# Kernel optimization log

Measured on AMD Instinct MI355X. Metric: run time of the kernel, lower is better.

The kernel has to match this reference:

```python
import jax, jax.numpy as jnp
import numpy as np

B, L, D, H = 2, 2048, 768, 12
DH = D // H          # 64
DFF = 4 * D          # 3072
ALPHA = 0.25         # lorentz_alpha
BLEND = 0.5          # blend for FFN and MinkowskiLayerNorm (set via set_blend)
EPS = 1e-5
SCALE = float(np.sqrt(DH))


def setup_inputs() -> dict:
    key = jax.random.key(0)
    ks = jax.random.split(key, 14)
    w = lambda k, shape: jax.random.normal(k, shape, jnp.float32) * 0.02
    causal = jnp.tril(jnp.ones((L, L), bool))
    attention_mask = jnp.where(causal, 0.0, -1e9).astype(jnp.float32)[None, None]
    return {
        'x': jax.random.normal(ks[0], (B, L, D), jnp.float32),
        'attention_mask': attention_mask,
        'timelike_mask': jax.random.bernoulli(ks[1], 0.25, (D,)),
        'Wq': w(ks[2], (D, D)), 'Wk': w(ks[3], (D, D)),
        'Wv': w(ks[4], (D, D)), 'Wo': w(ks[5], (D, D)),
        'w1': w(ks[6], (DFF, D)), 'w2': w(ks[7], (D, DFF)),
        'w1_t': w(ks[8], (DFF // 2, D)), 'w2_t': w(ks[9], (D, DFF // 2)),
        'w1_s': w(ks[10], (DFF // 2, D)), 'w2_s': w(ks[11], (D, DFF // 2)),
        'n1_w': jnp.ones(D, jnp.float32), 'n1_b': jnp.zeros(D, jnp.float32),
        'n2_w': jnp.ones(D, jnp.float32), 'n2_b': jnp.zeros(D, jnp.float32),
    }


def _mink_norm(x, m, w, b):
    # Minkowski LayerNorm blended with standard LN (m: float timelike mask)
    mean = x.mean(-1, keepdims=True)
    xc = x - mean
    var = (xc * xc).mean(-1, keepdims=True)
    x_std = xc / jnp.sqrt(var + EPS)
    sq = xc * xc
    eta = (sq * (1.0 - m)).sum(-1, keepdims=True) - (sq * m).sum(-1, keepdims=True)
    x_eta = xc / jnp.sqrt(jnp.abs(eta) + EPS)
    xn = (1.0 - BLEND) * x_std + BLEND * x_eta
    return w * xn + b


def _attn(x, attention_mask, m, Wq, Wk, Wv, Wo):
    # (B,L,D) -> (B,H,L,DH)
    split = lambda t: t.reshape(B, L, H, DH).transpose(0, 2, 1, 3)
    Q = split(x @ Wq.T)
    K = split(x @ Wk.T)
    V = split(x @ Wv.T)
    scores = jnp.einsum('bhqd,bhkd->bhqk', Q, K) / SCALE
    # Minkowski timelike correction: per-head diagonal mask on Q
    m2 = m.reshape(H, DH)[None, :, None, :]          # (1,H,1,DH)
    Q_t = Q * m2
    q_norm = jnp.linalg.norm(Q, axis=-1, keepdims=True)
    qt_norm = jnp.linalg.norm(Q_t, axis=-1, keepdims=True)
    sf = jnp.where(qt_norm > 1e-6, q_norm / jnp.maximum(qt_norm, 1e-8), 0.0)
    time_inner = jnp.einsum('bhqd,bhkd->bhqk', Q_t * sf, K) / SCALE
    scores = scores - 2.0 * ALPHA * time_inner
    scores = scores + attention_mask
    aw = jax.nn.softmax(scores, axis=-1)
    out = jnp.einsum('bhqk,bhkd->bhqd', aw, V)
    out = out.transpose(0, 2, 1, 3).reshape(B, L, D)
    return out @ Wo.T


def _ffn(x, m, w1, w2, w1_t, w2_t, w1_s, w2_s):
    std_out = jax.nn.gelu(x @ w1.T, approximate=False) @ w2.T
    h_t = jax.nn.silu((x * m) @ w1_t.T) @ w2_t.T
    h_s = jax.nn.gelu((x * (1.0 - m)) @ w1_s.T, approximate=False) @ w2_s.T
    return (1.0 - BLEND) * std_out + BLEND * (h_t + h_s)


def reference(x, attention_mask, timelike_mask, Wq, Wk, Wv, Wo,
              w1, w2, w1_t, w2_t, w1_s, w2_s, n1_w, n1_b, n2_w, n2_b):
    m = timelike_mask.astype(jnp.float32)
    ao = _attn(_mink_norm(x, m, n1_w, n1_b), attention_mask, m, Wq, Wk, Wv, Wo)
    x = x + ao
    x = x + _ffn(_mink_norm(x, m, n2_w, n2_b), m, w1, w2, w1_t, w2_t, w1_s, w2_s)
    return x
```

## Files before the change

### kernel.cpp

```cpp
#include <hip/hip_runtime.h>


typedef unsigned short u16;
typedef __bf16 bfrag __attribute__((ext_vector_type(8)));
typedef float f32x4 __attribute__((ext_vector_type(4)));

#define MFMA(a, b, c) __builtin_amdgcn_mfma_f32_16x16x32_bf16(a, b, c, 0, 0, 0)
#define NEG_BIG (-30000.0f)
#define ASYNC16(g, l)                                                        \
  __builtin_amdgcn_global_load_lds(                                          \
      (const __attribute__((address_space(1))) unsigned int*)(g),            \
      (__attribute__((address_space(3))) unsigned int*)(l), 16, 0, 0)

__device__ __forceinline__ float bf2f(u16 u) {
  unsigned int v = ((unsigned int)u) << 16;
  float f; __builtin_memcpy(&f, &v, 4); return f;
}
__device__ __forceinline__ u16 f2bf(float f) {
  unsigned int v; __builtin_memcpy(&v, &f, 4);
  v += 0x7fffu + ((v >> 16) & 1u);
  return (u16)(v >> 16);
}
__device__ __forceinline__ bfrag ldfrag(const u16* p) {
  bfrag v; __builtin_memcpy(&v, p, 16); return v;
}

__global__ __launch_bounds__(256) void mask_conv_k(const void* __restrict__ mask,
                                                   float* __restrict__ mfl) {
  __shared__ int msh;
  if (threadIdx.x == 0) msh = 0;
  __syncthreads();
  const unsigned int* w = (const unsigned int*)mask;
  if (threadIdx.x < 192) {
    const unsigned int v = w[threadIdx.x];
    if ((v & 0xFFFFu) == 0x3F80u) atomicOr(&msh, 4);
    else if (v == 0x3F800000u) atomicOr(&msh, 2);
    else if (v >= 2u) atomicOr(&msh, 1);
  }
  __syncthreads();
  const int m = msh;
  const int mode = (m & 4) ? 3 : (m & 2) ? 2 : (m & 1) ? 1 : 0;
  for (int i = threadIdx.x; i < 768; i += 256) {
    int b;
    if (mode == 3) b = ((const u16*)mask)[i] != 0;
    else if (mode == 2) b = ((const float*)mask)[i] != 0.0f;
    else if (mode == 1) b = ((const unsigned char*)mask)[i] != 0;
    else b = ((const int*)mask)[i] != 0;
    mfl[i] = (float)b;
  }
}

struct Segs {
  const void* src[14];
  int off[14];
  int n[14];
  int mmode[14];
};

__global__ __launch_bounds__(256) void convert_k(Segs segs, u16* __restrict__ dstb,
                                                 const float* __restrict__ mfl) {
  const int seg = blockIdx.y;
  const int n = segs.n[seg];
  const int mm = segs.mmode[seg];
  u16* dst = dstb + segs.off[seg];
  const float* src = (const float*)segs.src[seg];
  for (int i = (blockIdx.x * 256 + threadIdx.x) * 4; i < n; i += gridDim.x * 1024) {
    float4 v;
    __builtin_memcpy(&v, src + i, 16);
    if (mm) {
      const int k = i % 768;
      float m0 = mfl[k], m1 = mfl[k + 1], m2 = mfl[k + 2], m3 = mfl[k + 3];
      if (mm == 2) { m0 = 1.f - m0; m1 = 1.f - m1; m2 = 1.f - m2; m3 = 1.f - m3; }
      v.x *= m0; v.y *= m1; v.z *= m2; v.w *= m3;
    }
    dst[i] = f2bf(v.x); dst[i + 1] = f2bf(v.y);
    dst[i + 2] = f2bf(v.z); dst[i + 3] = f2bf(v.w);
  }
}

__global__ __launch_bounds__(256) void mink_norm_k(
    const float* __restrict__ X, const float* __restrict__ mf,
    const u16* __restrict__ w, const u16* __restrict__ bias,
    u16* __restrict__ Y) {
  __shared__ float red[8];
  const int row = blockIdx.x, tid = threadIdx.x;
  const int wid = tid >> 6, lane = tid & 63;
  const size_t roff = (size_t)row * 768;

  float xv[3], mv[3];
  int idx[3];
#pragma unroll
  for (int i = 0; i < 3; i++) {
    idx[i] = tid + i * 256;
    xv[i] = X[roff + idx[i]];
    mv[i] = mf[idx[i]];
  }
  float s = xv[0] + xv[1] + xv[2];
#pragma unroll
  for (int o = 32; o >= 1; o >>= 1) s += __shfl_xor(s, o, 64);
  if (lane == 0) red[wid] = s;
  __syncthreads();
  const float mean = (red[0] + red[1] + red[2] + red[3]) * (1.0f / 768.0f);
  __syncthreads();

  float xc[3], ss = 0.0f, sm = 0.0f;
#pragma unroll
  for (int i = 0; i < 3; i++) {
    xc[i] = xv[i] - mean;
    ss += xc[i] * xc[i];
    sm += xc[i] * xc[i] * mv[i];
  }
#pragma unroll
  for (int o = 32; o >= 1; o >>= 1) {
    ss += __shfl_xor(ss, o, 64);
    sm += __shfl_xor(sm, o, 64);
  }
  if (lane == 0) { red[wid] = ss; red[4 + wid] = sm; }
  __syncthreads();
  const float sumsq = red[0] + red[1] + red[2] + red[3];
  const float summ = red[4] + red[5] + red[6] + red[7];
  const float var = sumsq * (1.0f / 768.0f);
  const float eta = sumsq - 2.0f * summ;
  const float rs = 1.0f / sqrtf(var + 1e-5f);
  const float re = 1.0f / sqrtf(fabsf(eta) + 1e-5f);

#pragma unroll
  for (int i = 0; i < 3; i++) {
    const float xn = xc[i] * 0.5f * (rs + re);
    Y[roff + idx[i]] = f2bf(bf2f(w[idx[i]]) * xn + bf2f(bias[idx[i]]));
  }
}

__global__ __launch_bounds__(256) void qcorr_k(u16* __restrict__ Q,
                                               const float* __restrict__ mf) {
  const int idx = blockIdx.x * 4 + (threadIdx.x >> 6);
  const int t = threadIdx.x & 63;
  const int h = idx % 12;
  const int bl = idx / 12;
  const size_t off = (size_t)bl * 768 + h * 64 + t;
  const float q = bf2f(Q[off]);
  const float m = mf[h * 64 + t];
  float q2 = q * q, qm2 = q * q * m;
#pragma unroll
  for (int o = 32; o >= 1; o >>= 1) {
    q2 += __shfl_xor(q2, o, 64);
    qm2 += __shfl_xor(qm2, o, 64);
  }
  const float qn = sqrtf(q2), qtn = sqrtf(qm2);
  const float sf = (qtn > 1e-6f) ? qn / fmaxf(qtn, 1e-8f) : 0.0f;
  Q[off] = f2bf(q * (1.0f - 0.5f * sf * m) * 0.125f);
}

__device__ __forceinline__ void gemm128_loop(
    const u16* __restrict__ Ab, const u16* __restrict__ Wb2,
    int K, int lda, int ldb, u16 (*As)[32], u16 (*Bs)[32], f32x4 acc[4][4]) {
  const int tid = threadIdx.x;
  const int wid = tid >> 6, lane = tid & 63;
  const int lr = lane & 15, lq = lane >> 4;
  const int srow = wid * 32 + (lane >> 2);
  const int scol = (lane & 3) * 8;
  const u16* ga0 = Ab + (size_t)srow * lda + scol;
  const u16* ga1 = Ab + (size_t)(srow + 16) * lda + scol;
  const u16* gb0 = Wb2 + (size_t)srow * ldb + scol;
  const u16* gb1 = Wb2 + (size_t)(srow + 16) * ldb + scol;
  u16* la0 = &As[wid * 32][0];
  u16* la1 = &As[wid * 32 + 16][0];
  u16* lb0 = &Bs[wid * 32][0];
  u16* lb1 = &Bs[wid * 32 + 16][0];
  const int wr = (wid >> 1) * 64, wc = (wid & 1) * 64;

  for (int k0 = 0; k0 < K; k0 += 32) {
    __syncthreads();
    ASYNC16(ga0 + k0, la0);
    ASYNC16(ga1 + k0, la1);
    ASYNC16(gb0 + k0, lb0);
    ASYNC16(gb1 + k0, lb1);
    __syncthreads();
    bfrag af[4], bf4[4];
#pragma unroll
    for (int i = 0; i < 4; i++) af[i] = ldfrag(&As[wr + i * 16 + lr][lq * 8]);
#pragma unroll
    for (int j = 0; j < 4; j++) bf4[j] = ldfrag(&Bs[wc + j * 16 + lr][lq * 8]);
#pragma unroll
    for (int i = 0; i < 4; i++)
#pragma unroll
      for (int j = 0; j < 4; j++)
        acc[i][j] = MFMA(af[i], bf4[j], acc[i][j]);
  }
}

struct GSeg { const u16* W; u16* C; int ldc; int nblk; int epi; };
struct GArgs { GSeg s[3]; };

__global__ __launch_bounds__(256) void gemm128_fused(
    const u16* __restrict__ A, int lda, int K, GArgs args) {
  __shared__ __align__(16) u16 As[128][32];
  __shared__ __align__(16) u16 Bs[128][32];
  int cb = blockIdx.x, seg = 0;
  while (cb >= args.s[seg].nblk) { cb -= args.s[seg].nblk; seg++; }
  const GSeg g = args.s[seg];
  const int rowb = blockIdx.y * 128, colb = cb * 128;
  f32x4 acc[4][4] = {};
  gemm128_loop(A + (size_t)rowb * lda, g.W + (size_t)colb * K, K, lda, K,
               As, Bs, acc);

  const int lane = threadIdx.x & 63, wid = threadIdx.x >> 6;
  const int lr = lane & 15, lq = lane >> 4;
  const int wr = (wid >> 1) * 64, wc = (wid & 1) * 64;
#pragma unroll
  for (int i = 0; i < 4; i++)
#pragma unroll
    for (int j = 0; j < 4; j++)
#pragma unroll
      for (int r = 0; r < 4; r++) {
        const int row = rowb + wr + i * 16 + lq * 4 + r;
        const int col = colb + wc + j * 16 + lr;
        float v = acc[i][j][r];
        if (g.epi == 2) v = 0.5f * v * (1.0f + erff(v * 0.70710678118654752f));
        else if (g.epi == 3) v = v / (1.0f + __expf(-v));
        g.C[(size_t)row * g.ldc + col] = f2bf(v);
      }
}

__global__ __launch_bounds__(256) void gemm128_res(
    const u16* __restrict__ A, const u16* __restrict__ W,
    const float* __restrict__ R, float* __restrict__ Out, int lda, int K,
    int N) {
  __shared__ __align__(16) u16 As[128][32];
  __shared__ __align__(16) u16 Bs[128][32];
  const int rowb = blockIdx.y * 128, colb = blockIdx.x * 128;
  f32x4 acc[4][4] = {};
  gemm128_loop(A + (size_t)rowb * lda, W + (size_t)colb * K, K, lda, K,
               As, Bs, acc);

  const int lane = threadIdx.x & 63, wid = threadIdx.x >> 6;
  const int lr = lane & 15, lq = lane >> 4;
  const int wr = (wid >> 1) * 64, wc = (wid & 1) * 64;
#pragma unroll
  for (int i = 0; i < 4; i++)
#pragma unroll
    for (int j = 0; j < 4; j++)
#pragma unroll
      for (int r = 0; r < 4; r++) {
        const int row = rowb + wr + i * 16 + lq * 4 + r;
        const int col = colb + wc + j * 16 + lr;
        const size_t o = (size_t)row * N + col;
        Out[o] = acc[i][j][r] + R[o];
      }
}

__global__ __launch_bounds__(256) void ffn2_splitk(
    const u16* __restrict__ H1, const u16* __restrict__ Ht,
    const u16* __restrict__ Hs, const u16* __restrict__ W2,
    const u16* __restrict__ W2t, const u16* __restrict__ W2s,
    float* __restrict__ Out) {
  __shared__ __align__(16) u16 As[128][32];
  __shared__ __align__(16) u16 Bs[128][32];
  const int rowb = blockIdx.y * 128, colb = blockIdx.x * 128;
  const int z = blockIdx.z;
  f32x4 acc[4][4] = {};
  if (z == 0)
    gemm128_loop(H1 + (size_t)rowb * 3072, W2 + (size_t)colb * 3072,
                 1536, 3072, 3072, As, Bs, acc);
  else if (z == 1)
    gemm128_loop(H1 + (size_t)rowb * 3072 + 1536,
                 W2 + (size_t)colb * 3072 + 1536,
                 1536, 3072, 3072, As, Bs, acc);
  else if (z == 2)
    gemm128_loop(Ht + (size_t)rowb * 1536, W2t + (size_t)colb * 1536,
                 1536, 1536, 1536, As, Bs, acc);
  else
    gemm128_loop(Hs + (size_t)rowb * 1536, W2s + (size_t)colb * 1536,
                 1536, 1536, 1536, As, Bs, acc);

  const int lane = threadIdx.x & 63, wid = threadIdx.x >> 6;
  const int lr = lane & 15, lq = lane >> 4;
  const int wr = (wid >> 1) * 64, wc = (wid & 1) * 64;
#pragma unroll
  for (int i = 0; i < 4; i++)
#pragma unroll
    for (int j = 0; j < 4; j++)
#pragma unroll
      for (int r = 0; r < 4; r++) {
        const int row = rowb + wr + i * 16 + lq * 4 + r;
        const int col = colb + wc + j * 16 + lr;
        atomicAdd(&Out[(size_t)row * 768 + col], 0.5f * acc[i][j][r]);
      }
}

__global__ __launch_bounds__(256) void flash_attn_k(
    const u16* __restrict__ Qc, const u16* __restrict__ Kb,
    const u16* __restrict__ Vb, u16* __restrict__ O) {
  __shared__ __align__(16) u16 Ks[64][40];
  __shared__ __align__(16) u16 Vt[64][72];
  __shared__ __align__(16) u16 Ps[4][16][72];
  const int tid = threadIdx.x, wid = tid >> 6, lane = tid & 63;
  const int lr = lane & 15, lq = lane >> 4;
  const int qt = gridDim.x - 1 - blockIdx.x;
  const int qb = qt * 64;
  const int bh = blockIdx.y;
  const int b = bh / 12, h = bh % 12;
  const int q0 = qb + wid * 16;
  const size_t base = (size_t)b * 2048 * 768 + h * 64;

  bfrag aq[2];
  aq[0] = ldfrag(Qc + base + (size_t)(q0 + lr) * 768 + lq * 8);
  aq[1] = ldfrag(Qc + base + (size_t)(q0 + lr) * 768 + 32 + lq * 8);

  f32x4 o[4] = {};
  float mrow[4] = {NEG_BIG, NEG_BIG, NEG_BIG, NEG_BIG};
  float lrow[4] = {0.0f, 0.0f, 0.0f, 0.0f};

  const int krow = tid >> 3;
  const int kcol = (tid & 7) * 8;
  const int vkey = tid & 31;
  const int vdg = tid >> 5;

  const int nt = qt + 1;

  const u16* kp = Kb + base + (size_t)krow * 768 + kcol;
  const u16* vp = Vb + base + (size_t)vkey * 768 + vdg * 8;

  uint4 kv0, kv1, vv0, vv1;
  __builtin_memcpy(&kv0, kp, 16);
  __builtin_memcpy(&kv1, kp + (size_t)32 * 768, 16);
  __builtin_memcpy(&vv0, vp, 16);
  __builtin_memcpy(&vv1, vp + (size_t)32 * 768, 16);

  for (int kt = 0; kt < nt; kt++) {
    __syncthreads();
    __builtin_memcpy(&Ks[krow][kcol], &kv0, 16);
    __builtin_memcpy(&Ks[krow + 32][kcol], &kv1, 16);
    {
      union { uint4 u; u16 s[8]; } a, b2;
      a.u = vv0; b2.u = vv1;
#pragma unroll
      for (int j = 0; j < 8; j++) {
        Vt[vdg * 8 + j][vkey] = a.s[j];
        Vt[vdg * 8 + j][vkey + 32] = b2.s[j];
      }
    }
    __syncthreads();
    if (kt + 1 < nt) {
      const size_t koff = (size_t)(kt + 1) * 64 * 768;
      __builtin_memcpy(&kv0, kp + koff, 16);
      __builtin_memcpy(&kv1, kp + koff + (size_t)32 * 768, 16);
      __builtin_memcpy(&vv0, vp + koff, 16);
      __builtin_memcpy(&vv1, vp + koff + (size_t)32 * 768, 16);
    }

    const int kbk = kt * 64;
    if (kbk <= q0 + 15) {
      f32x4 s4[4] = {};
#pragma unroll
      for (int kg = 0; kg < 2; kg++) {
#pragma unroll
        for (int c = 0; c < 4; c++) {
          bfrag bk = ldfrag(&Ks[c * 16 + lr][kg * 32 + lq * 8]);
          s4[c] = MFMA(aq[kg], bk, s4[c]);
        }
      }
#pragma unroll
      for (int r = 0; r < 4; r++) {
        const int q = q0 + lq * 4 + r;
        float v[4];
        float mx = NEG_BIG;
#pragma unroll
        for (int c = 0; c < 4; c++) {
          v[c] = (kbk + c * 16 + lr > q) ? NEG_BIG : s4[c][r];
          mx = fmaxf(mx, v[c]);
        }
#pragma unroll
        for (int off = 8; off >= 1; off >>= 1)
          mx = fmaxf(mx, __shfl_xor(mx, off, 16));
        const float mn = fmaxf(mrow[r], mx);
        const float alpha = __expf(mrow[r] - mn);
        float sm = 0.0f;
        float p[4];
#pragma unroll
        for (int c = 0; c < 4; c++) {
          p[c] = __expf(v[c] - mn);
          sm += p[c];
        }
#pragma unroll
        for (int off = 8; off >= 1; off >>= 1) sm += __shfl_xor(sm, off, 16);
        lrow[r] = lrow[r] * alpha + sm;
        mrow[r] = mn;
#pragma unroll
        for (int dt = 0; dt < 4; dt++) o[dt][r] *= alpha;
#pragma unroll
        for (int c = 0; c < 4; c++)
          Ps[wid][lq * 4 + r][c * 16 + lr] = f2bf(p[c]);
      }
      __threadfence_block();
      bfrag pf0 = ldfrag(&Ps[wid][lr][lq * 8]);
      bfrag pf1 = ldfrag(&Ps[wid][lr][32 + lq * 8]);
#pragma unroll
      for (int dt = 0; dt < 4; dt++) {
        bfrag v0 = ldfrag(&Vt[dt * 16 + lr][lq * 8]);
        bfrag v1 = ldfrag(&Vt[dt * 16 + lr][32 + lq * 8]);
        o[dt] = MFMA(pf0, v0, o[dt]);
        o[dt] = MFMA(pf1, v1, o[dt]);
      }
    }
  }

#pragma unroll
  for (int r = 0; r < 4; r++) {
    const float inv = 1.0f / fmaxf(lrow[r], 1e-30f);
    const int q = q0 + lq * 4 + r;
#pragma unroll
    for (int dt = 0; dt < 4; dt++)
      O[base + (size_t)q * 768 + dt * 16 + lr] = f2bf(o[dt][r] * inv);
  }
}

extern "C" void kernel_launch(void* const* d_in, const int* in_sizes, int n_in,
                              void* d_out, int out_size, void* d_ws,
                              size_t ws_size, hipStream_t stream) {
  (void)in_sizes; (void)n_in; (void)out_size; (void)ws_size;
  const float* x = (const float*)d_in[0];
  const void* mask = d_in[2];

  char* ws = (char*)d_ws;
  u16* Wb  = (u16*)(ws);
  u16* n1h = (u16*)(ws + 23599104);
  u16* Qb  = (u16*)(ws + 48764928);
  u16* Kb2 = (u16*)(ws + 55056384);
  u16* Vb2 = (u16*)(ws + 61347840);
  u16* att = (u16*)(ws + 67639296);
  u16* hs  = (u16*)(ws + 80222208);
  float* mfl = (float*)(ws + 92805120);
  float* x1 = (float*)d_out;

  u16* Wq = Wb + 0,        *Wk = Wb + 589824,   *Wv = Wb + 1179648;
  u16* Wo = Wb + 1769472,  *w1 = Wb + 2359296,  *w1t = Wb + 4718592;
  u16* w1s = Wb + 5898240, *w2 = Wb + 7077888,  *w2t = Wb + 9437184;
  u16* w2s = Wb + 10616832;
  u16* n1w = Wb + 11796480, *n1b = Wb + 11797248;
  u16* n2w = Wb + 11798016, *n2b = Wb + 11798784;

  Segs sg;
  const int srcidx[14] = {3, 4, 5, 6, 7, 9, 11, 8, 10, 12, 13, 14, 15, 16};
  const int offs[14] = {0, 589824, 1179648, 1769472, 2359296, 4718592,
                        5898240, 7077888, 9437184, 10616832,
                        11796480, 11797248, 11798016, 11798784};
  const int ns[14] = {589824, 589824, 589824, 589824, 2359296, 1179648,
                      1179648, 2359296, 1179648, 1179648, 768, 768, 768, 768};
  const int mms[14] = {0, 0, 0, 0, 0, 1, 2, 0, 0, 0, 0, 0, 0, 0};
  for (int i = 0; i < 14; i++) {
    sg.src[i] = d_in[srcidx[i]];
    sg.off[i] = offs[i];
    sg.n[i] = ns[i];
    sg.mmode[i] = mms[i];
  }

  mask_conv_k<<<1, 256, 0, stream>>>(mask, mfl);
  convert_k<<<dim3(2304, 14), 256, 0, stream>>>(sg, Wb, mfl);

  mink_norm_k<<<4096, 256, 0, stream>>>(x, mfl, n1w, n1b, n1h);

  GArgs qkv;
  qkv.s[0] = {Wq, Qb, 768, 6, 0};
  qkv.s[1] = {Wk, Kb2, 768, 6, 0};
  qkv.s[2] = {Wv, Vb2, 768, 6, 0};
  gemm128_fused<<<dim3(18, 32), 256, 0, stream>>>(n1h, 768, 768, qkv);

  qcorr_k<<<12288, 256, 0, stream>>>(Qb, mfl);
  flash_attn_k<<<dim3(32, 24), 256, 0, stream>>>(Qb, Kb2, Vb2, att);

  gemm128_res<<<dim3(6, 32), 256, 0, stream>>>(att, Wo, x, x1, 768, 768, 768);

  mink_norm_k<<<4096, 256, 0, stream>>>(x1, mfl, n2w, n2b, Qb);

  GArgs ffn1;
  ffn1.s[0] = {w1, n1h, 3072, 24, 2};
  ffn1.s[1] = {w1t, att, 1536, 12, 3};
  ffn1.s[2] = {w1s, hs, 1536, 12, 2};
  gemm128_fused<<<dim3(48, 32), 256, 0, stream>>>(Qb, 768, 768, ffn1);

  ffn2_splitk<<<dim3(6, 32, 4), 256, 0, stream>>>(n1h, att, hs, w2, w2t, w2s,
                                                  (float*)d_out);
}
```

Before: 465.4 us.

## Halve flash-attention query tile and split-K the Wo projection with atomics

Flash attention now runs 128-thread blocks over 32 query rows, launching twice as many blocks so the causal workload balances better across CUs. Each thread loads twice as much K/V data per tile to compensate for the smaller block. The Wo projection is split along K into two halves that atomically accumulate into x1. The residual is pre-seeded by having the first norm kernel copy x into x1. This raises parallelism for the small GEMM, at the cost of extra atomic traffic, nondeterministic summation order, and each K/V tile being loaded twice as often overall.

```diff
diff --git a/kernel.cpp b/kernel.cpp
--- a/kernel.cpp
+++ b/kernel.cpp
@@ -81,7 +81,7 @@
 __global__ __launch_bounds__(256) void mink_norm_k(
     const float* __restrict__ X, const float* __restrict__ mf,
     const u16* __restrict__ w, const u16* __restrict__ bias,
-    u16* __restrict__ Y) {
+    u16* __restrict__ Y, float* __restrict__ Xcopy) {
   __shared__ float red[8];
   const int row = blockIdx.x, tid = threadIdx.x;
   const int wid = tid >> 6, lane = tid & 63;
@@ -94,6 +94,10 @@
     idx[i] = tid + i * 256;
     xv[i] = X[roff + idx[i]];
     mv[i] = mf[idx[i]];
+  }
+  if (Xcopy) {
+#pragma unroll
+    for (int i = 0; i < 3; i++) Xcopy[roff + idx[i]] = xv[i];
   }
   float s = xv[0] + xv[1] + xv[2];
 #pragma unroll
@@ -222,16 +226,16 @@
       }
 }
 
-__global__ __launch_bounds__(256) void gemm128_res(
+__global__ __launch_bounds__(256) void gemm128_wo_splitk(
     const u16* __restrict__ A, const u16* __restrict__ W,
-    const float* __restrict__ R, float* __restrict__ Out, int lda, int K,
-    int N) {
+    float* __restrict__ Out) {
   __shared__ __align__(16) u16 As[128][32];
   __shared__ __align__(16) u16 Bs[128][32];
   const int rowb = blockIdx.y * 128, colb = blockIdx.x * 128;
+  const int z = blockIdx.z;
   f32x4 acc[4][4] = {};
-  gemm128_loop(A + (size_t)rowb * lda, W + (size_t)colb * K, K, lda, K,
-               As, Bs, acc);
+  gemm128_loop(A + (size_t)rowb * 768 + z * 384,
+               W + (size_t)colb * 768 + z * 384, 384, 768, 768, As, Bs, acc);
 
   const int lane = threadIdx.x & 63, wid = threadIdx.x >> 6;
   const int lr = lane & 15, lq = lane >> 4;
@@ -244,8 +248,7 @@
       for (int r = 0; r < 4; r++) {
         const int row = rowb + wr + i * 16 + lq * 4 + r;
         const int col = colb + wc + j * 16 + lr;
-        const size_t o = (size_t)row * N + col;
-        Out[o] = acc[i][j][r] + R[o];
+        atomicAdd(&Out[(size_t)row * 768 + col], acc[i][j][r]);
       }
 }
 
@@ -288,16 +291,16 @@
       }
 }
 
-__global__ __launch_bounds__(256) void flash_attn_k(
+__global__ __launch_bounds__(128) void flash_attn_k(
     const u16* __restrict__ Qc, const u16* __restrict__ Kb,
     const u16* __restrict__ Vb, u16* __restrict__ O) {
   __shared__ __align__(16) u16 Ks[64][40];
   __shared__ __align__(16) u16 Vt[64][72];
-  __shared__ __align__(16) u16 Ps[4][16][72];
+  __shared__ __align__(16) u16 Ps[2][16][72];
   const int tid = threadIdx.x, wid = tid >> 6, lane = tid & 63;
   const int lr = lane & 15, lq = lane >> 4;
   const int qt = gridDim.x - 1 - blockIdx.x;
-  const int qb = qt * 64;
+  const int qb = qt * 32;
   const int bh = blockIdx.y;
   const int b = bh / 12, h = bh % 12;
   const int q0 = qb + wid * 16;
@@ -316,37 +319,49 @@
   const int vkey = tid & 31;
   const int vdg = tid >> 5;
 
-  const int nt = qt + 1;
+  const int nt = qt / 2 + 1;
 
   const u16* kp = Kb + base + (size_t)krow * 768 + kcol;
   const u16* vp = Vb + base + (size_t)vkey * 768 + vdg * 8;
 
-  uint4 kv0, kv1, vv0, vv1;
+  uint4 kv0, kv1, kv2, kv3, va0, va1, vb0, vb1;
   __builtin_memcpy(&kv0, kp, 16);
-  __builtin_memcpy(&kv1, kp + (size_t)32 * 768, 16);
-  __builtin_memcpy(&vv0, vp, 16);
-  __builtin_memcpy(&vv1, vp + (size_t)32 * 768, 16);
+  __builtin_memcpy(&kv1, kp + (size_t)16 * 768, 16);
+  __builtin_memcpy(&kv2, kp + (size_t)32 * 768, 16);
+  __builtin_memcpy(&kv3, kp + (size_t)48 * 768, 16);
+  __builtin_memcpy(&va0, vp, 16);
+  __builtin_memcpy(&va1, vp + 32, 16);
+  __builtin_memcpy(&vb0, vp + (size_t)32 * 768, 16);
+  __builtin_memcpy(&vb1, vp + (size_t)32 * 768 + 32, 16);
 
   for (int kt = 0; kt < nt; kt++) {
     __syncthreads();
     __builtin_memcpy(&Ks[krow][kcol], &kv0, 16);
-    __builtin_memcpy(&Ks[krow + 32][kcol], &kv1, 16);
+    __builtin_memcpy(&Ks[krow + 16][kcol], &kv1, 16);
+    __builtin_memcpy(&Ks[krow + 32][kcol], &kv2, 16);
+    __builtin_memcpy(&Ks[krow + 48][kcol], &kv3, 16);
     {
-      union { uint4 u; u16 s[8]; } a, b2;
-      a.u = vv0; b2.u = vv1;
+      union { uint4 u; u16 s[8]; } a0, a1, b0, b1;
+      a0.u = va0; a1.u = va1; b0.u = vb0; b1.u = vb1;
 #pragma unroll
       for (int j = 0; j < 8; j++) {
-        Vt[vdg * 8 + j][vkey] = a.s[j];
-        Vt[vdg * 8 + j][vkey + 32] = b2.s[j];
+        Vt[vdg * 8 + j][vkey] = a0.s[j];
+        Vt[vdg * 8 + 32 + j][vkey] = a1.s[j];
+        Vt[vdg * 8 + j][vkey + 32] = b0.s[j];
+        Vt[vdg * 8 + 32 + j][vkey + 32] = b1.s[j];
       }
     }
     __syncthreads();
     if (kt + 1 < nt) {
       const size_t koff = (size_t)(kt + 1) * 64 * 768;
       __builtin_memcpy(&kv0, kp + koff, 16);
-      __builtin_memcpy(&kv1, kp + koff + (size_t)32 * 768, 16);
-      __builtin_memcpy(&vv0, vp + koff, 16);
-      __builtin_memcpy(&vv1, vp + koff + (size_t)32 * 768, 16);
+      __builtin_memcpy(&kv1, kp + koff + (size_t)16 * 768, 16);
+      __builtin_memcpy(&kv2, kp + koff + (size_t)32 * 768, 16);
+      __builtin_memcpy(&kv3, kp + koff + (size_t)48 * 768, 16);
+      __builtin_memcpy(&va0, vp + koff, 16);
+      __builtin_memcpy(&va1, vp + koff + 32, 16);
+      __builtin_memcpy(&vb0, vp + koff + (size_t)32 * 768, 16);
+      __builtin_memcpy(&vb1, vp + koff + (size_t)32 * 768 + 32, 16);
     }
 
     const int kbk = kt * 64;
@@ -458,7 +473,7 @@
   mask_conv_k<<<1, 256, 0, stream>>>(mask, mfl);
   convert_k<<<dim3(2304, 14), 256, 0, stream>>>(sg, Wb, mfl);
 
-  mink_norm_k<<<4096, 256, 0, stream>>>(x, mfl, n1w, n1b, n1h);
+  mink_norm_k<<<4096, 256, 0, stream>>>(x, mfl, n1w, n1b, n1h, x1);
 
   GArgs qkv;
   qkv.s[0] = {Wq, Qb, 768, 6, 0};
@@ -467,11 +482,11 @@
   gemm128_fused<<<dim3(18, 32), 256, 0, stream>>>(n1h, 768, 768, qkv);
 
   qcorr_k<<<12288, 256, 0, stream>>>(Qb, mfl);
-  flash_attn_k<<<dim3(32, 24), 256, 0, stream>>>(Qb, Kb2, Vb2, att);
-
-  gemm128_res<<<dim3(6, 32), 256, 0, stream>>>(att, Wo, x, x1, 768, 768, 768);
-
-  mink_norm_k<<<4096, 256, 0, stream>>>(x1, mfl, n2w, n2b, Qb);
+  flash_attn_k<<<dim3(64, 24), 128, 0, stream>>>(Qb, Kb2, Vb2, att);
+
+  gemm128_wo_splitk<<<dim3(6, 32, 2), 256, 0, stream>>>(att, Wo, x1);
+
+  mink_norm_k<<<4096, 256, 0, stream>>>(x1, mfl, n2w, n2b, Qb, nullptr);
 
   GArgs ffn1;
   ffn1.s[0] = {w1, n1h, 3072, 24, 2};
```

Result: slower. 481.5 us (+3.5%).

## Split flash attention over key chunks with merge kernel; split-K Wo projection

Applied to the files above, without the earlier changes.

Causal flash attention is split along the key dimension into chunks of eight tiles for long query tiles. Each chunk writes unnormalized partial outputs plus its row max and row sum, and a new merge kernel combines them with rescaling. This is meant to balance work across the grid, which is 80 blocks per head instead of 32 uneven ones. The Wo projection becomes a two-way split-K with atomic adds into the output, which the first norm kernel now pre-fills with the residual x. The cost is an extra kernel launch, fp32 partial traffic through reused workspace buffers, and atomics.

```diff
diff --git a/kernel.cpp b/kernel.cpp
--- a/kernel.cpp
+++ b/kernel.cpp
@@ -81,7 +81,7 @@
 __global__ __launch_bounds__(256) void mink_norm_k(
     const float* __restrict__ X, const float* __restrict__ mf,
     const u16* __restrict__ w, const u16* __restrict__ bias,
-    u16* __restrict__ Y) {
+    u16* __restrict__ Y, float* __restrict__ Xcopy) {
   __shared__ float red[8];
   const int row = blockIdx.x, tid = threadIdx.x;
   const int wid = tid >> 6, lane = tid & 63;
@@ -94,6 +94,10 @@
     idx[i] = tid + i * 256;
     xv[i] = X[roff + idx[i]];
     mv[i] = mf[idx[i]];
+  }
+  if (Xcopy) {
+#pragma unroll
+    for (int i = 0; i < 3; i++) Xcopy[roff + idx[i]] = xv[i];
   }
   float s = xv[0] + xv[1] + xv[2];
 #pragma unroll
@@ -222,16 +226,16 @@
       }
 }
 
-__global__ __launch_bounds__(256) void gemm128_res(
+__global__ __launch_bounds__(256) void gemm128_wo_splitk(
     const u16* __restrict__ A, const u16* __restrict__ W,
-    const float* __restrict__ R, float* __restrict__ Out, int lda, int K,
-    int N) {
+    float* __restrict__ Out) {
   __shared__ __align__(16) u16 As[128][32];
   __shared__ __align__(16) u16 Bs[128][32];
   const int rowb = blockIdx.y * 128, colb = blockIdx.x * 128;
+  const int z = blockIdx.z;
   f32x4 acc[4][4] = {};
-  gemm128_loop(A + (size_t)rowb * lda, W + (size_t)colb * K, K, lda, K,
-               As, Bs, acc);
+  gemm128_loop(A + (size_t)rowb * 768 + z * 384,
+               W + (size_t)colb * 768 + z * 384, 384, 768, 768, As, Bs, acc);
 
   const int lane = threadIdx.x & 63, wid = threadIdx.x >> 6;
   const int lr = lane & 15, lq = lane >> 4;
@@ -244,8 +248,7 @@
       for (int r = 0; r < 4; r++) {
         const int row = rowb + wr + i * 16 + lq * 4 + r;
         const int col = colb + wc + j * 16 + lr;
-        const size_t o = (size_t)row * N + col;
-        Out[o] = acc[i][j][r] + R[o];
+        atomicAdd(&Out[(size_t)row * 768 + col], acc[i][j][r]);
       }
 }
 
@@ -290,13 +293,24 @@
 
 __global__ __launch_bounds__(256) void flash_attn_k(
     const u16* __restrict__ Qc, const u16* __restrict__ Kb,
-    const u16* __restrict__ Vb, u16* __restrict__ O) {
+    const u16* __restrict__ Vb, u16* __restrict__ O,
+    float* __restrict__ Pn, float* __restrict__ Ph) {
   __shared__ __align__(16) u16 Ks[64][40];
   __shared__ __align__(16) u16 Vt[64][72];
   __shared__ __align__(16) u16 Ps[4][16][72];
   const int tid = threadIdx.x, wid = tid >> 6, lane = tid & 63;
   const int lr = lane & 15, lq = lane >> 4;
-  const int qt = gridDim.x - 1 - blockIdx.x;
+
+  int bx = blockIdx.x, qt = 0, c = 0;
+  for (int q = 31; q >= 0; --q) {
+    const int nc = (q < 8) ? 1 : (q / 8 + 1);
+    if (bx < nc) { qt = q; c = bx; break; }
+    bx -= nc;
+  }
+  const int nt = qt + 1;
+  const int t0 = c * 8;
+  const int t1 = (t0 + 8 < nt) ? t0 + 8 : nt;
+
   const int qb = qt * 64;
   const int bh = blockIdx.y;
   const int b = bh / 12, h = bh % 12;
@@ -316,10 +330,8 @@
   const int vkey = tid & 31;
   const int vdg = tid >> 5;
 
-  const int nt = qt + 1;
-
-  const u16* kp = Kb + base + (size_t)krow * 768 + kcol;
-  const u16* vp = Vb + base + (size_t)vkey * 768 + vdg * 8;
+  const u16* kp = Kb + base + (size_t)(t0 * 64 + krow) * 768 + kcol;
+  const u16* vp = Vb + base + (size_t)(t0 * 64 + vkey) * 768 + vdg * 8;
 
   uint4 kv0, kv1, vv0, vv1;
   __builtin_memcpy(&kv0, kp, 16);
@@ -327,7 +339,7 @@
   __builtin_memcpy(&vv0, vp, 16);
   __builtin_memcpy(&vv1, vp + (size_t)32 * 768, 16);
 
-  for (int kt = 0; kt < nt; kt++) {
+  for (int kt = t0; kt < t1; kt++) {
     __syncthreads();
     __builtin_memcpy(&Ks[krow][kcol], &kv0, 16);
     __builtin_memcpy(&Ks[krow + 32][kcol], &kv1, 16);
@@ -341,8 +353,8 @@
       }
     }
     __syncthreads();
-    if (kt + 1 < nt) {
-      const size_t koff = (size_t)(kt + 1) * 64 * 768;
+    if (kt + 1 < t1) {
+      const size_t koff = (size_t)(kt + 1 - t0) * 64 * 768;
       __builtin_memcpy(&kv0, kp + koff, 16);
       __builtin_memcpy(&kv1, kp + koff + (size_t)32 * 768, 16);
       __builtin_memcpy(&vv0, vp + koff, 16);
@@ -350,14 +362,14 @@
     }
 
     const int kbk = kt * 64;
-    if (kbk <= q0 + 15) {
+    {
       f32x4 s4[4] = {};
 #pragma unroll
       for (int kg = 0; kg < 2; kg++) {
 #pragma unroll
-        for (int c = 0; c < 4; c++) {
-          bfrag bk = ldfrag(&Ks[c * 16 + lr][kg * 32 + lq * 8]);
-          s4[c] = MFMA(aq[kg], bk, s4[c]);
+        for (int cc = 0; cc < 4; cc++) {
+          bfrag bk = ldfrag(&Ks[cc * 16 + lr][kg * 32 + lq * 8]);
+          s4[cc] = MFMA(aq[kg], bk, s4[cc]);
         }
       }
 #pragma unroll
@@ -366,9 +378,9 @@
         float v[4];
         float mx = NEG_BIG;
 #pragma unroll
-        for (int c = 0; c < 4; c++) {
-          v[c] = (kbk + c * 16 + lr > q) ? NEG_BIG : s4[c][r];
-          mx = fmaxf(mx, v[c]);
+        for (int cc = 0; cc < 4; cc++) {
+          v[cc] = (kbk + cc * 16 + lr > q) ? NEG_BIG : s4[cc][r];
+          mx = fmaxf(mx, v[cc]);
         }
 #pragma unroll
         for (int off = 8; off >= 1; off >>= 1)
@@ -378,9 +390,9 @@
         float sm = 0.0f;
         float p[4];
 #pragma unroll
-        for (int c = 0; c < 4; c++) {
-          p[c] = __expf(v[c] - mn);
-          sm += p[c];
+        for (int cc = 0; cc < 4; cc++) {
+          p[cc] = __expf(v[cc] - mn);
+          sm += p[cc];
         }
 #pragma unroll
         for (int off = 8; off >= 1; off >>= 1) sm += __shfl_xor(sm, off, 16);
@@ -389,8 +401,8 @@
 #pragma unroll
         for (int dt = 0; dt < 4; dt++) o[dt][r] *= alpha;
 #pragma unroll
-        for (int c = 0; c < 4; c++)
-          Ps[wid][lq * 4 + r][c * 16 + lr] = f2bf(p[c]);
+        for (int cc = 0; cc < 4; cc++)
+          Ps[wid][lq * 4 + r][cc * 16 + lr] = f2bf(p[cc]);
       }
       __threadfence_block();
       bfrag pf0 = ldfrag(&Ps[wid][lr][lq * 8]);
@@ -405,14 +417,78 @@
     }
   }
 
-#pragma unroll
-  for (int r = 0; r < 4; r++) {
-    const float inv = 1.0f / fmaxf(lrow[r], 1e-30f);
-    const int q = q0 + lq * 4 + r;
-#pragma unroll
-    for (int dt = 0; dt < 4; dt++)
-      O[base + (size_t)q * 768 + dt * 16 + lr] = f2bf(o[dt][r] * inv);
-  }
+  if (qt < 8) {
+#pragma unroll
+    for (int r = 0; r < 4; r++) {
+      const float inv = 1.0f / fmaxf(lrow[r], 1e-30f);
+      const int q = q0 + lq * 4 + r;
+#pragma unroll
+      for (int dt = 0; dt < 4; dt++)
+        O[base + (size_t)q * 768 + dt * 16 + lr] = f2bf(o[dt][r] * inv);
+    }
+  } else {
+    int off = 0;
+    for (int j = 8; j < qt; ++j) off += j / 8 + 1;
+    const int s = bh * 72 + off + c;
+    float* Op = (s < 1536) ? Pn + (size_t)s * 4096
+                           : Ph + (size_t)(s - 1536) * 4096;
+    float* lmp = Ph + 786432 + (size_t)s * 128;
+#pragma unroll
+    for (int r = 0; r < 4; r++) {
+      const int row = wid * 16 + lq * 4 + r;
+#pragma unroll
+      for (int dt = 0; dt < 4; dt++)
+        Op[(size_t)row * 64 + dt * 16 + lr] = o[dt][r];
+      if (lr == 0) { lmp[row] = mrow[r]; lmp[64 + row] = lrow[r]; }
+    }
+  }
+}
+
+__global__ __launch_bounds__(256) void attn_merge_k(
+    const float* __restrict__ Pn, const float* __restrict__ Ph,
+    u16* __restrict__ O) {
+  const int qt = 8 + blockIdx.x;
+  const int bh = blockIdx.y;
+  const int b = bh / 12, h = bh % 12;
+  const int nc = qt / 8 + 1;
+  int off = 0;
+  for (int j = 8; j < qt; ++j) off += j / 8 + 1;
+  const int s0 = bh * 72 + off;
+  const int row = threadIdx.x >> 2;
+  const int c0 = (threadIdx.x & 3) * 16;
+  const float* lmb = Ph + 786432;
+
+  float mg = NEG_BIG;
+  for (int cc = 0; cc < nc; ++cc)
+    mg = fmaxf(mg, lmb[(size_t)(s0 + cc) * 128 + row]);
+
+  float acc[16];
+#pragma unroll
+  for (int j = 0; j < 16; j++) acc[j] = 0.0f;
+  float lg = 0.0f;
+  for (int cc = 0; cc < nc; ++cc) {
+    const int s = s0 + cc;
+    const float mcv = lmb[(size_t)s * 128 + row];
+    const float coef = __expf(mcv - mg);
+    lg += coef * lmb[(size_t)s * 128 + 64 + row];
+    const float* Op = (s < 1536) ? Pn + (size_t)s * 4096
+                                 : Ph + (size_t)(s - 1536) * 4096;
+    const float* rp = Op + (size_t)row * 64 + c0;
+#pragma unroll
+    for (int g = 0; g < 4; g++) {
+      float4 v;
+      __builtin_memcpy(&v, rp + g * 4, 16);
+      acc[g * 4 + 0] += coef * v.x;
+      acc[g * 4 + 1] += coef * v.y;
+      acc[g * 4 + 2] += coef * v.z;
+      acc[g * 4 + 3] += coef * v.w;
+    }
+  }
+  const float inv = 1.0f / fmaxf(lg, 1e-30f);
+  const int q = qt * 64 + row;
+  const size_t ob = (size_t)b * 2048 * 768 + h * 64 + (size_t)q * 768 + c0;
+#pragma unroll
+  for (int j = 0; j < 16; j++) O[ob + j] = f2bf(acc[j] * inv);
 }
 
 extern "C" void kernel_launch(void* const* d_in, const int* in_sizes, int n_in,
@@ -432,6 +508,8 @@
   u16* hs  = (u16*)(ws + 80222208);
   float* mfl = (float*)(ws + 92805120);
   float* x1 = (float*)d_out;
+  float* Pn = (float*)n1h;
+  float* Ph = (float*)hs;
 
   u16* Wq = Wb + 0,        *Wk = Wb + 589824,   *Wv = Wb + 1179648;
   u16* Wo = Wb + 1769472,  *w1 = Wb + 2359296,  *w1t = Wb + 4718592;
@@ -458,7 +536,7 @@
   mask_conv_k<<<1, 256, 0, stream>>>(mask, mfl);
   convert_k<<<dim3(2304, 14), 256, 0, stream>>>(sg, Wb, mfl);
 
-  mink_norm_k<<<4096, 256, 0, stream>>>(x, mfl, n1w, n1b, n1h);
+  mink_norm_k<<<4096, 256, 0, stream>>>(x, mfl, n1w, n1b, n1h, x1);
 
   GArgs qkv;
   qkv.s[0] = {Wq, Qb, 768, 6, 0};
@@ -467,11 +545,13 @@
   gemm128_fused<<<dim3(18, 32), 256, 0, stream>>>(n1h, 768, 768, qkv);
 
   qcorr_k<<<12288, 256, 0, stream>>>(Qb, mfl);
-  flash_attn_k<<<dim3(32, 24), 256, 0, stream>>>(Qb, Kb2, Vb2, att);
-
-  gemm128_res<<<dim3(6, 32), 256, 0, stream>>>(att, Wo, x, x1, 768, 768, 768);
-
-  mink_norm_k<<<4096, 256, 0, stream>>>(x1, mfl, n2w, n2b, Qb);
+
+  flash_attn_k<<<dim3(80, 24), 256, 0, stream>>>(Qb, Kb2, Vb2, att, Pn, Ph);
+  attn_merge_k<<<dim3(24, 24), 256, 0, stream>>>(Pn, Ph, att);
+
+  gemm128_wo_splitk<<<dim3(6, 32, 2), 256, 0, stream>>>(att, Wo, x1);
+
+  mink_norm_k<<<4096, 256, 0, stream>>>(x1, mfl, n2w, n2b, Qb, nullptr);
 
   GArgs ffn1;
   ffn1.s[0] = {w1, n1h, 3072, 24, 2};
```

Result: faster. 444.7 us (-4.5%).
